# Optimization experiments

Measured on AMD Instinct MI355X. Metric: run time of the kernel, lower is better.

## Reference

```python
import jax, jax.numpy as jnp
import numpy as np

N_TOKENS = 3
EMBED = 10
RNN = 10
N_LABELS = 3
B = 16384
T = 99
EPS = 1e-7  # keras CategoricalCrossentropy clip epsilon


def setup_inputs() -> dict:
    key = jax.random.key(0)
    ks = jax.random.split(key, 8)
    token_ids = jax.random.randint(ks[0], (B, T), 0, N_TOKENS, dtype=jnp.int32)
    label_ids = jax.random.randint(ks[1], (B, T), 0, N_LABELS)
    labels = jax.nn.one_hot(label_ids, N_LABELS, dtype=jnp.float32)
    mask = jnp.ones((B, T), dtype=bool)  # accepted by call() but unused, kept for signature fidelity
    emb_table = jax.random.normal(ks[2], (N_TOKENS, EMBED), jnp.float32) * 0.05
    W = jax.random.normal(ks[3], (EMBED, RNN), jnp.float32) / np.sqrt(EMBED)
    U = jax.random.normal(ks[4], (RNN, RNN), jnp.float32) / np.sqrt(RNN)
    b = jnp.zeros((RNN,), jnp.float32)
    Wo = jax.random.normal(ks[5], (RNN, N_LABELS), jnp.float32) / np.sqrt(RNN)
    bo = jnp.zeros((N_LABELS,), jnp.float32)
    return dict(token_ids=token_ids, labels=labels, mask=mask,
                emb_table=emb_table, W=W, U=U, b=b, Wo=Wo, bo=bo)


def reference(token_ids, labels, mask, emb_table, W, U, b, Wo, bo):
    # Embedding lookup (mask_zero=True -> token 0 is a masked step)
    emb = emb_table[token_ids]                      # [B, T, E]
    step_mask = (token_ids != 0)                    # [B, T]

    def step(h, inp):
        x_t, m_t = inp                              # [B, E], [B]
        h_new = jnp.tanh(x_t @ W + h @ U + b)       # SimpleRNN cell
        # Keras masking: masked timesteps carry previous state/output
        h = jnp.where(m_t[:, None], h_new, h)
        return h, h

    h0 = jnp.zeros((token_ids.shape[0], W.shape[1]), emb.dtype)
    _, states_tb = jax.lax.scan(step, h0, (emb.transpose(1, 0, 2), step_mask.T))
    states = states_tb.transpose(1, 0, 2)           # [B, T, R]

    probs = jax.nn.softmax(states @ Wo + bo, axis=-1)   # Dense(softmax) -> [B, T, L]
    probs_c = jnp.clip(probs, EPS, 1.0)
    loss = jnp.mean(-jnp.sum(labels * jnp.log(probs_c), axis=-1))
    accuracy = jnp.mean((jnp.argmax(probs, axis=-1) == jnp.argmax(labels, axis=-1)).astype(jnp.float32))
    return states, probs, accuracy, loss
```

## Files before the change

kernel.cpp:

```cpp
#include <hip/hip_runtime.h>
#include <math.h>

#define BB 16384
#define TT 99
#define RR 10
#define LL 3
#define TILE 33

__device__ __forceinline__ float fast_tanh(float x) {
    float e = __expf(2.0f * x);
    return fmaf(-2.0f, __builtin_amdgcn_rcpf(e + 1.0f), 1.0f);
}

__global__ __launch_bounds__(256, 2)
void rnn_fused_kernel(const int* __restrict__ tok_ids,
                      const float* __restrict__ labels,
                      const float* __restrict__ emb,
                      const float* __restrict__ W,
                      const float* __restrict__ U,
                      const float* __restrict__ bvec,
                      const float* __restrict__ Wo,
                      const float* __restrict__ bo,
                      float* __restrict__ states_out,
                      float* __restrict__ probs_out,
                      float* __restrict__ ws)
{
    __shared__ __align__(16) float          s_st[4][8 * TILE * RR];
    __shared__                unsigned char s_tk[4][8 * 100];

    const int tid = threadIdx.x;
    const int w   = tid >> 6;
    const int l   = tid & 63;
    const int r8  = l >> 3;
    const int g   = l & 7;
    const int rb  = l & 56;
    const int rowbase = blockIdx.x * 32 + w * 8;

#pragma unroll
    for (int i = 0; i < 13; ++i) {
        const int q = l + 64 * i;
        if (q < 8 * TT) {
            const int tk = tok_ids[(size_t)rowbase * TT + q];
            const int r  = q / TT;
            s_tk[w][q + r] = (unsigned char)tk;
        }
    }

    const int jg0 = g;
    const int jg1 = (g < 2) ? 8 + g : g;
    float U0[RR], U1[RR];
    float c10 = bvec[jg0], c20 = c10;
    float c11 = bvec[jg1], c21 = c11;
#pragma unroll
    for (int i = 0; i < RR; ++i) {
        U0[i] = U[i * RR + jg0];
        U1[i] = U[i * RR + jg1];
        const float w0 = W[i * RR + jg0];
        const float w1 = W[i * RR + jg1];
        c10 = fmaf(emb[RR + i],     w0, c10);
        c20 = fmaf(emb[2 * RR + i], w0, c20);
        c11 = fmaf(emb[RR + i],     w1, c11);
        c21 = fmaf(emb[2 * RR + i], w1, c21);
    }

    float ho0 = 0.0f, ho1 = 0.0f;
    float loss = 0.0f;
    int   corr = 0;
    int sel = (int)s_tk[w][r8 * 100 + 0];

#pragma unroll 1
    for (int k = 0; k < 3; ++k) {
#pragma unroll 1
        for (int tt = 0; tt < TILE; ++tt) {
            const int t   = k * TILE + tt;
            const int cur = sel;
            const int tn  = (t + 1 < TT) ? t + 1 : t;
            sel = (int)s_tk[w][r8 * 100 + tn];

            float h[RR];
#pragma unroll
            for (int i = 0; i < 8; ++i) h[i] = __shfl(ho0, rb + i, 64);
            h[8] = __shfl(ho1, rb + 0, 64);
            h[9] = __shfl(ho1, rb + 1, 64);

            float a0 = (cur == 1) ? c10 : c20;
            float a1 = (cur == 1) ? c11 : c21;
#pragma unroll
            for (int i = 0; i < RR; ++i) {
                a0 = fmaf(h[i], U0[i], a0);
                a1 = fmaf(h[i], U1[i], a1);
            }
            const float hn0 = fast_tanh(a0);
            const float hn1 = fast_tanh(a1);
            if (cur != 0) { ho0 = hn0; ho1 = hn1; }

            float* sp = &s_st[w][r8 * (TILE * RR) + tt * RR];
            sp[g] = ho0;
            if (g < 2) sp[8 + g] = ho1;
        }

        const int    t0 = k * TILE;
        const size_t gb = (size_t)rowbase * (TT * RR) + (size_t)k * (TILE * RR);

#pragma unroll
        for (int i = 0; i < 21; ++i) {
            const int q = l + 64 * i;
            if (q < 1320) {
                const int r = q / 165;
                const int m = q - r * 165;
                const float2 v = *reinterpret_cast<const float2*>(
                    &s_st[w][r * (TILE * RR) + 2 * m]);
                *reinterpret_cast<float2*>(
                    &states_out[gb + (size_t)r * (TT * RR) + 2 * m]) = v;
            }
        }

#pragma unroll
        for (int i = 0; i < 5; ++i) {
            const int p = l + 64 * i;
            if (p < 8 * TILE) {
                const int r  = p / TILE;
                const int tt = p - r * TILE;
                const size_t idx = (size_t)(rowbase + r) * TT + t0 + tt;

                const float* hp = &s_st[w][r * (TILE * RR) + tt * RR];
                float l0 = bo[0], l1 = bo[1], l2 = bo[2];
#pragma unroll
                for (int j = 0; j < RR; ++j) {
                    const float hj = hp[j];
                    l0 = fmaf(hj, Wo[j * LL + 0], l0);
                    l1 = fmaf(hj, Wo[j * LL + 1], l1);
                    l2 = fmaf(hj, Wo[j * LL + 2], l2);
                }
                const float e0 = __expf(l0), e1 = __expf(l1), e2 = __expf(l2);
                const float S  = e0 + e1 + e2;
                const float rs = __builtin_amdgcn_rcpf(S);
                probs_out[idx * LL + 0] = e0 * rs;
                probs_out[idx * LL + 1] = e1 * rs;
                probs_out[idx * LL + 2] = e2 * rs;

                const float la1 = labels[idx * LL + 1];
                const float la2 = labels[idx * LL + 2];
                const int   y   = (la1 > 0.5f) ? 1 : ((la2 > 0.5f) ? 2 : 0);

                const float ly = (y == 0) ? l0 : ((y == 1) ? l1 : l2);
                loss += fminf(__logf(S) - ly, 16.11809565f);

                int ap = 0; float pm = l0;
                if (l1 > pm) { ap = 1; pm = l1; }
                if (l2 > pm) { ap = 2; }
                corr += (ap == y) ? 1 : 0;
            }
        }
    }

    float ls = loss, cs = (float)corr;
#pragma unroll
    for (int off = 32; off > 0; off >>= 1) {
        ls += __shfl_down(ls, off, 64);
        cs += __shfl_down(cs, off, 64);
    }
    if (l == 0) {
        const int wid = blockIdx.x * 4 + w;
        ws[wid]        = ls;
        ws[2048 + wid] = cs;
    }
}

__global__ __launch_bounds__(256)
void finalize_kernel(const float* __restrict__ ws, float* __restrict__ out_tail)
{
    __shared__ float sl[4], sc[4];
    const int t = threadIdx.x;
    float ls = 0.0f, cs = 0.0f;
#pragma unroll
    for (int i = 0; i < 8; ++i) {
        ls += ws[t + 256 * i];
        cs += ws[2048 + t + 256 * i];
    }
#pragma unroll
    for (int off = 32; off > 0; off >>= 1) {
        ls += __shfl_down(ls, off, 64);
        cs += __shfl_down(cs, off, 64);
    }
    if ((t & 63) == 0) { sl[t >> 6] = ls; sc[t >> 6] = cs; }
    __syncthreads();
    if (t == 0) {
        const float L = sl[0] + sl[1] + sl[2] + sl[3];
        const float C = sc[0] + sc[1] + sc[2] + sc[3];
        const float inv = 1.0f / (float)((size_t)BB * TT);
        out_tail[0] = C * inv;
        out_tail[1] = L * inv;
    }
}

extern "C" void kernel_launch(void* const* d_in, const int* in_sizes, int n_in,
                              void* d_out, int out_size, void* d_ws, size_t ws_size,
                              hipStream_t stream)
{
    const int*   tok    = (const int*)  d_in[0];
    const float* labels = (const float*)d_in[1];
    const float* emb = (const float*)d_in[3];
    const float* W   = (const float*)d_in[4];
    const float* U   = (const float*)d_in[5];
    const float* bv  = (const float*)d_in[6];
    const float* Wo  = (const float*)d_in[7];
    const float* bo  = (const float*)d_in[8];

    float* out    = (float*)d_out;
    float* states = out;
    float* probs  = out + (size_t)BB * TT * RR;
    float* tail   = out + (size_t)BB * TT * (RR + LL);
    float* ws     = (float*)d_ws;

    rnn_fused_kernel<<<BB / 32, 256, 0, stream>>>(tok, labels, emb, W, U, bv, Wo, bo,
                                                  states, probs, ws);
    finalize_kernel<<<1, 256, 0, stream>>>(ws, tail);
}
```

Measured before the change: 50.10 us.

## Map 16 rows per wave with 4 lanes per row and DPP broadcasts

Each wave now handles 16 batch rows instead of 8, with 4 lanes per row each computing 3 hidden units, so the grid shrinks to 256 blocks. Hidden-state exchange uses row-local DPP quad broadcasts instead of cross-lane shuffles. Labels are read and packed with the token ids up front, so the softmax/loss phase takes the label from shared memory. This cuts shuffle latency in the serial recurrence and makes label loads coalesced up front, but it doubles shared memory per block, lowers occupancy to one block per CU, and uses only 256 blocks, which may underfill the GPU.

```diff
diff --git a/kernel.cpp b/kernel.cpp
--- a/kernel.cpp
+++ b/kernel.cpp
@@ -6,13 +6,18 @@
 #define RR 10
 #define LL 3
 #define TILE 33
+#define RPW 16
+#define WPB 4
+
+#define QPB(v, Q) __int_as_float(__builtin_amdgcn_mov_dpp(                    \
+    __float_as_int(v), (Q) * 0x55, 0xF, 0xF, true))
 
 __device__ __forceinline__ float fast_tanh(float x) {
     float e = __expf(2.0f * x);
     return fmaf(-2.0f, __builtin_amdgcn_rcpf(e + 1.0f), 1.0f);
 }
 
-__global__ __launch_bounds__(256, 2)
+__global__ __launch_bounds__(256, 1)
 void rnn_fused_kernel(const int* __restrict__ tok_ids,
                       const float* __restrict__ labels,
                       const float* __restrict__ emb,
@@ -25,105 +30,121 @@
                       float* __restrict__ probs_out,
                       float* __restrict__ ws)
 {
-    __shared__ __align__(16) float          s_st[4][8 * TILE * RR];
-    __shared__                unsigned char s_tk[4][8 * 100];
+    __shared__ __align__(16) float          s_st[WPB][RPW * TILE * RR];
+    __shared__                unsigned char s_code[WPB][RPW * 100];
 
     const int tid = threadIdx.x;
     const int w   = tid >> 6;
     const int l   = tid & 63;
-    const int r8  = l >> 3;
-    const int g   = l & 7;
-    const int rb  = l & 56;
-    const int rowbase = blockIdx.x * 32 + w * 8;
-
-#pragma unroll
-    for (int i = 0; i < 13; ++i) {
-        const int q = l + 64 * i;
-        if (q < 8 * TT) {
-            const int tk = tok_ids[(size_t)rowbase * TT + q];
-            const int r  = q / TT;
-            s_tk[w][q + r] = (unsigned char)tk;
-        }
-    }
-
-    const int jg0 = g;
-    const int jg1 = (g < 2) ? 8 + g : g;
-    float U0[RR], U1[RR];
-    float c10 = bvec[jg0], c20 = c10;
-    float c11 = bvec[jg1], c21 = c11;
+    const int r4  = l >> 2;
+    const int q   = l & 3;
+    const int rowbase = blockIdx.x * (WPB * RPW) + w * RPW;
+
+#pragma unroll 1
+    for (int g = 0; g < 5; ++g) {
+#pragma unroll
+        for (int u = 0; u < 5; ++u) {
+            const int p = l + 64 * (g * 5 + u);
+            if (p < RPW * TT) {
+                const size_t gi = (size_t)rowbase * TT + p;
+                const int   tk  = tok_ids[gi];
+                const float la1 = labels[gi * LL + 1];
+                const float la2 = labels[gi * LL + 2];
+                const int   y   = (la1 > 0.5f) ? 1 : ((la2 > 0.5f) ? 2 : 0);
+                const int   r   = p / TT;
+                s_code[w][r * 100 + (p - r * TT)] = (unsigned char)((tk << 2) | y);
+            }
+        }
+    }
+
+    const int uA = q;
+    const int uB = 4 + q;
+    const int uC = (q < 2) ? 8 + q : q;
+    float UA[RR], UB[RR], UC[RR];
+    float cA1 = bvec[uA], cA2 = cA1;
+    float cB1 = bvec[uB], cB2 = cB1;
+    float cC1 = bvec[uC], cC2 = cC1;
 #pragma unroll
     for (int i = 0; i < RR; ++i) {
-        U0[i] = U[i * RR + jg0];
-        U1[i] = U[i * RR + jg1];
-        const float w0 = W[i * RR + jg0];
-        const float w1 = W[i * RR + jg1];
-        c10 = fmaf(emb[RR + i],     w0, c10);
-        c20 = fmaf(emb[2 * RR + i], w0, c20);
-        c11 = fmaf(emb[RR + i],     w1, c11);
-        c21 = fmaf(emb[2 * RR + i], w1, c21);
-    }
-
-    float ho0 = 0.0f, ho1 = 0.0f;
+        UA[i] = U[i * RR + uA];
+        UB[i] = U[i * RR + uB];
+        UC[i] = U[i * RR + uC];
+        const float wA = W[i * RR + uA];
+        const float wB = W[i * RR + uB];
+        const float wC = W[i * RR + uC];
+        const float e1 = emb[RR + i];
+        const float e2 = emb[2 * RR + i];
+        cA1 = fmaf(e1, wA, cA1); cA2 = fmaf(e2, wA, cA2);
+        cB1 = fmaf(e1, wB, cB1); cB2 = fmaf(e2, wB, cB2);
+        cC1 = fmaf(e1, wC, cC1); cC2 = fmaf(e2, wC, cC2);
+    }
+
+    float hoA = 0.0f, hoB = 0.0f, hoC = 0.0f;
     float loss = 0.0f;
     int   corr = 0;
-    int sel = (int)s_tk[w][r8 * 100 + 0];
+    int code = (int)s_code[w][r4 * 100];
 
 #pragma unroll 1
     for (int k = 0; k < 3; ++k) {
 #pragma unroll 1
         for (int tt = 0; tt < TILE; ++tt) {
             const int t   = k * TILE + tt;
-            const int cur = sel;
+            const int cur = code;
             const int tn  = (t + 1 < TT) ? t + 1 : t;
-            sel = (int)s_tk[w][r8 * 100 + tn];
+            code = (int)s_code[w][r4 * 100 + tn];
+            const int sel = cur >> 2;
 
             float h[RR];
-#pragma unroll
-            for (int i = 0; i < 8; ++i) h[i] = __shfl(ho0, rb + i, 64);
-            h[8] = __shfl(ho1, rb + 0, 64);
-            h[9] = __shfl(ho1, rb + 1, 64);
-
-            float a0 = (cur == 1) ? c10 : c20;
-            float a1 = (cur == 1) ? c11 : c21;
+            h[0] = QPB(hoA, 0); h[1] = QPB(hoA, 1);
+            h[2] = QPB(hoA, 2); h[3] = QPB(hoA, 3);
+            h[4] = QPB(hoB, 0); h[5] = QPB(hoB, 1);
+            h[6] = QPB(hoB, 2); h[7] = QPB(hoB, 3);
+            h[8] = QPB(hoC, 0); h[9] = QPB(hoC, 1);
+
+            const bool is1 = (sel == 1);
+            float aA = is1 ? cA1 : cA2;
+            float aB = is1 ? cB1 : cB2;
+            float aC = is1 ? cC1 : cC2;
 #pragma unroll
             for (int i = 0; i < RR; ++i) {
-                a0 = fmaf(h[i], U0[i], a0);
-                a1 = fmaf(h[i], U1[i], a1);
-            }
-            const float hn0 = fast_tanh(a0);
-            const float hn1 = fast_tanh(a1);
-            if (cur != 0) { ho0 = hn0; ho1 = hn1; }
-
-            float* sp = &s_st[w][r8 * (TILE * RR) + tt * RR];
-            sp[g] = ho0;
-            if (g < 2) sp[8 + g] = ho1;
-        }
-
-        const int    t0 = k * TILE;
-        const size_t gb = (size_t)rowbase * (TT * RR) + (size_t)k * (TILE * RR);
-
-#pragma unroll
-        for (int i = 0; i < 21; ++i) {
-            const int q = l + 64 * i;
-            if (q < 1320) {
-                const int r = q / 165;
-                const int m = q - r * 165;
+                aA = fmaf(h[i], UA[i], aA);
+                aB = fmaf(h[i], UB[i], aB);
+                aC = fmaf(h[i], UC[i], aC);
+            }
+            const float hnA = fast_tanh(aA);
+            const float hnB = fast_tanh(aB);
+            const float hnC = fast_tanh(aC);
+            if (sel != 0) { hoA = hnA; hoB = hnB; hoC = hnC; }
+
+            float* sp = &s_st[w][(r4 * TILE + tt) * RR];
+            sp[q]     = hoA;
+            sp[4 + q] = hoB;
+            if (q < 2) sp[8 + q] = hoC;
+        }
+
+#pragma unroll
+        for (int i = 0; i < 42; ++i) {
+            const int p = l + 64 * i;
+            if (p < RPW * TILE * RR / 2) {
+                const int r = p / 165;
+                const int m = p - r * 165;
                 const float2 v = *reinterpret_cast<const float2*>(
                     &s_st[w][r * (TILE * RR) + 2 * m]);
                 *reinterpret_cast<float2*>(
-                    &states_out[gb + (size_t)r * (TT * RR) + 2 * m]) = v;
-            }
-        }
-
-#pragma unroll
-        for (int i = 0; i < 5; ++i) {
+                    &states_out[(size_t)(rowbase + r) * (TT * RR)
+                                + (size_t)k * (TILE * RR) + 2 * m]) = v;
+            }
+        }
+
+#pragma unroll
+        for (int i = 0; i < 9; ++i) {
             const int p = l + 64 * i;
-            if (p < 8 * TILE) {
+            if (p < RPW * TILE) {
                 const int r  = p / TILE;
-                const int tt = p - r * TILE;
-                const size_t idx = (size_t)(rowbase + r) * TT + t0 + tt;
-
-                const float* hp = &s_st[w][r * (TILE * RR) + tt * RR];
+                const int t2 = p - r * TILE;
+                const size_t idx = (size_t)(rowbase + r) * TT + k * TILE + t2;
+
+                const float* hp = &s_st[w][(r * TILE + t2) * RR];
                 float l0 = bo[0], l1 = bo[1], l2 = bo[2];
 #pragma unroll
                 for (int j = 0; j < RR; ++j) {
@@ -139,9 +160,7 @@
                 probs_out[idx * LL + 1] = e1 * rs;
                 probs_out[idx * LL + 2] = e2 * rs;
 
-                const float la1 = labels[idx * LL + 1];
-                const float la2 = labels[idx * LL + 2];
-                const int   y   = (la1 > 0.5f) ? 1 : ((la2 > 0.5f) ? 2 : 0);
+                const int y = (int)s_code[w][r * 100 + k * TILE + t2] & 3;
 
                 const float ly = (y == 0) ? l0 : ((y == 1) ? l1 : l2);
                 loss += fminf(__logf(S) - ly, 16.11809565f);
@@ -161,9 +180,9 @@
         cs += __shfl_down(cs, off, 64);
     }
     if (l == 0) {
-        const int wid = blockIdx.x * 4 + w;
+        const int wid = blockIdx.x * WPB + w;
         ws[wid]        = ls;
-        ws[2048 + wid] = cs;
+        ws[1024 + wid] = cs;
     }
 }
 
@@ -174,9 +193,9 @@
     const int t = threadIdx.x;
     float ls = 0.0f, cs = 0.0f;
 #pragma unroll
-    for (int i = 0; i < 8; ++i) {
+    for (int i = 0; i < 4; ++i) {
         ls += ws[t + 256 * i];
-        cs += ws[2048 + t + 256 * i];
+        cs += ws[1024 + t + 256 * i];
     }
 #pragma unroll
     for (int off = 32; off > 0; off >>= 1) {
@@ -213,7 +232,7 @@
     float* tail   = out + (size_t)BB * TT * (RR + LL);
     float* ws     = (float*)d_ws;
 
-    rnn_fused_kernel<<<BB / 32, 256, 0, stream>>>(tok, labels, emb, W, U, bv, Wo, bo,
-                                                  states, probs, ws);
+    rnn_fused_kernel<<<BB / (WPB * RPW), 256, 0, stream>>>(
+        tok, labels, emb, W, U, bv, Wo, bo, states, probs, ws);
     finalize_kernel<<<1, 256, 0, stream>>>(ws, tail);
 }
```

Result: slower. 52.22 us (+4.2%).
